# Performance work log

Measured on AMD Instinct MI355X. Metric: run time of the kernel, lower is better.

Reference implementation:

```python
import jax, jax.numpy as jnp
import numpy as np

ALPHA1 = 0.1
ALPHA2 = 0.1
NOISE = 0.02
B, T, H, O = 128, 512, 512, 3


def setup_inputs() -> dict:
    key = jax.random.key(0)
    ks = jax.random.split(key, 10)
    return {
        "x": jax.random.normal(ks[0], (B, T, 5), dtype=jnp.float32),
        "wi_stim": jax.random.normal(ks[1], (3, H), dtype=jnp.float32) / np.sqrt(3),
        "wrec11": jax.random.normal(ks[2], (H, H), dtype=jnp.float32) / np.sqrt(H),
        "wi_ctx": jax.random.normal(ks[3], (2, H), dtype=jnp.float32) / np.sqrt(2),
        "wrec22": jax.random.normal(ks[4], (H, H), dtype=jnp.float32) / np.sqrt(H),
        "wrec12": jax.random.normal(ks[5], (H, H), dtype=jnp.float32) / np.sqrt(H),
        "wrec21": jax.random.normal(ks[6], (H, H), dtype=jnp.float32) / np.sqrt(H),
        "wo": jax.random.normal(ks[7], (H, O), dtype=jnp.float32) / np.sqrt(H),
        "noise1": jax.random.normal(ks[8], (T, B, H), dtype=jnp.float32),
        "noise2": jax.random.normal(ks[9], (T, B, H), dtype=jnp.float32),
    }


def reference(x, wi_stim, wrec11, wi_ctx, wrec22, wrec12, wrec21, wo, noise1, noise2):
    # x: [B, T, 5]; noise: [T, B, H] (pre-sampled standard normals, scaled by NOISE)
    xs = jnp.transpose(x[:, :, :3], (1, 0, 2))  # [T, B, 3]
    xc = jnp.transpose(x[:, :, 3:], (1, 0, 2))  # [T, B, 2]

    def step(carry, inp):
        h1, h2 = carry
        xsi, xci, n1, n2 = inp
        h1 = (1 - ALPHA1) * h1 + ALPHA1 * (
            xsi @ wi_stim + jnp.tanh(h1) @ wrec11 + jnp.tanh(h2) @ wrec12 + n1 * NOISE
        )
        # note: h2 update uses the freshly-updated h1 (as in the torch loop)
        h2 = (1 - ALPHA2) * h2 + ALPHA2 * (
            xci @ wi_ctx + jnp.tanh(h1) @ wrec21 + jnp.tanh(h2) @ wrec22 + n2 * NOISE
        )
        return (h1, h2), jnp.tanh(h2) @ wo

    h0 = jnp.zeros((x.shape[0], wrec11.shape[0]), dtype=x.dtype)
    _, out_t = jax.lax.scan(step, (h0, h0), (xs, xc, noise1, noise2))  # [T, B, O]
    return jnp.transpose(out_t, (1, 0, 2))  # [B, T, O]
```

## Files before the change

kernel.cpp:

```cpp
#include <hip/hip_runtime.h>
#include <hip/hip_bf16.h>

#define TT 512
#define BB 128
#define HH 512
#define NGROUP 8
#define NSLICE 8
#define ALPHA 0.1f
#define NOISE_S 0.02f

typedef __attribute__((ext_vector_type(8))) short short8;
typedef __attribute__((ext_vector_type(8))) _Float16 half8;
typedef __attribute__((ext_vector_type(4))) float f32x4;

#define WPACK_CH 132096
#define PUB1_B (WPACK_CH * 16)
#define PUB2_B (PUB1_B + NGROUP * 16384)
#define FLAG_B (PUB2_B + NGROUP * 16384)

__device__ __forceinline__ unsigned short f2h(float f) {
  return __builtin_bit_cast(unsigned short, (_Float16)f);
}

__device__ __forceinline__ float fast_tanh(float x) {
  float e = __builtin_amdgcn_exp2f(x * 2.8853900817779268f);
  return 1.0f - 2.0f * __builtin_amdgcn_rcpf(e + 1.0f);
}

__device__ __forceinline__ f32x4 mfma16(short8 a, short8 b, f32x4 c) {
  return __builtin_amdgcn_mfma_f32_16x16x32_f16(
      __builtin_bit_cast(half8, a), __builtin_bit_cast(half8, b), c, 0, 0, 0);
}

__global__ void pack_weights(const float* __restrict__ w11, const float* __restrict__ w12,
                             const float* __restrict__ w21, const float* __restrict__ w22,
                             const float* __restrict__ wo, unsigned short* __restrict__ dst) {
  int idx = blockIdx.x * 256 + threadIdx.x;
  if (idx < 131072) {
    int which = idx >> 16;
    int c0 = idx & 65535;
    int kt = c0 >> 11, rem = c0 & 2047;
    int nt = rem >> 6, lane = rem & 63;
    const float* wlo = which ? w21 : w11;
    const float* whi = which ? w22 : w12;
    unsigned short* p = dst + (size_t)idx * 8;
    int n = nt * 16 + (lane & 15);
    int kb = kt * 32 + ((lane >> 4) & 3) * 8;
#pragma unroll
    for (int i = 0; i < 8; ++i) {
      int k = kb + i;
      float v = (k < HH) ? wlo[k * HH + n] : whi[(k - HH) * HH + n];
      p[i] = f2h(v);
    }
  } else if (idx < 132096) {
    int c0 = idx - 131072;
    int kt = c0 >> 6, lane = c0 & 63;
    unsigned short* p = dst + (size_t)131072 * 8 + (size_t)c0 * 8;
    int n = lane & 15;
    int kb = kt * 32 + ((lane >> 4) & 3) * 8;
#pragma unroll
    for (int i = 0; i < 8; ++i) {
      float v = (n < 3) ? wo[(kb + i) * 3 + n] : 0.0f;
      p[i] = f2h(v);
    }
  }
}

__global__ void zero_ws(int* __restrict__ p, int n) {
  for (int i = blockIdx.x * 256 + threadIdx.x; i < n; i += gridDim.x * 256)
    p[i] = 0;
}

__global__ __launch_bounds__(256, 1)
void rnn_main(const float* __restrict__ x, const float* __restrict__ wi_stim,
              const float* __restrict__ wi_ctx, const float* __restrict__ noise1,
              const float* __restrict__ noise2, char* __restrict__ ws,
              float* __restrict__ out) {
  __shared__ __align__(16) unsigned short T1buf[16 * 512];
  __shared__ __align__(16) unsigned short T2buf[16 * 512];
  __shared__ __align__(16) unsigned short WOlds[16 * 512];
  __shared__ float xstage[2][16][5];

  const int tid = threadIdx.x;
  const int w = tid >> 6, lane = tid & 63;
  const int c16 = lane & 15, kh = lane >> 4;
  const int g = blockIdx.x & (NGROUP - 1);
  const int slice = blockIdx.x >> 3;
  const int nt = slice * 4 + w;
  const int n0 = nt * 16;
  const int b0 = g * 16;
  const int lrow0 = kh * 4;

  const short8* __restrict__ WC = (const short8*)ws;
  unsigned short* __restrict__ pub1 = (unsigned short*)(ws + PUB1_B) + g * 8192;
  unsigned short* __restrict__ pub2 = (unsigned short*)(ws + PUB2_B) + g * 8192;
  int* __restrict__ fl1 = (int*)(ws + FLAG_B) + g * 8;
  int* __restrict__ fl2 = (int*)(ws + FLAG_B) + NGROUP * 8 + g * 8;

  short8 z = {0, 0, 0, 0, 0, 0, 0, 0};
  for (int i = tid; i < 1024; i += 256) {
    ((short8*)T1buf)[i] = z;
    ((short8*)T2buf)[i] = z;
  }
#pragma unroll
  for (int c = 0; c < 4; ++c) {
    int kt = w * 4 + c;
    short8 v = WC[131072 + kt * 64 + lane];
    *(short8*)&WOlds[kt * 512 + lane * 8] = v;
  }
  if (tid < 80) {
    int b = tid / 5, c = tid % 5;
    xstage[0][b][c] = x[((size_t)(b0 + b) * TT + 0) * 5 + c];
  }

  float wis[3], wic[2];
#pragma unroll
  for (int c = 0; c < 3; ++c) wis[c] = wi_stim[c * HH + n0 + c16];
#pragma unroll
  for (int c = 0; c < 2; ++c) wic[c] = wi_ctx[c * HH + n0 + c16];

  float h1[4] = {0, 0, 0, 0}, h2[4] = {0, 0, 0, 0};

  const int kt_p = nt >> 1;
  const int hi = (((nt & 1) * 16) + c16) >> 3;
  const int ci = c16 & 7;

  const short8* __restrict__ WAp = WC + nt * 64 + lane;
  const short8* __restrict__ WBp = WC + 65536 + nt * 64 + lane;

  auto poll = [&](int* f, int target) {
    int v;
    do {
      v = (lane < 8) ? __hip_atomic_load(&f[lane], __ATOMIC_RELAXED,
                                         __HIP_MEMORY_SCOPE_AGENT)
                     : target;
    } while (!__all(v >= target));
    __builtin_amdgcn_sched_barrier(0);
    asm volatile("" ::: "memory");
  };

  __syncthreads();

  for (int t = 0; t < TT; ++t) {
    const int buf = t & 1;

    float n1v[4];
#pragma unroll
    for (int r = 0; r < 4; ++r)
      n1v[r] = noise1[((size_t)t * BB + b0 + lrow0 + r) * HH + n0 + c16];

    f32x4 aA = {0, 0, 0, 0}, aB = {0, 0, 0, 0};
#pragma unroll
    for (int kt = 0; kt < 16; ++kt) {
      short8 a1 = *(const short8*)&T1buf[kt * 512 + lane * 8];
      aA = mfma16(a1, WAp[kt * 2048], aA);
    }
    poll(fl2, t);
#pragma unroll
    for (int c = 0; c < 4; ++c) {
      int kt = w * 4 + c;
      const unsigned long long* src =
          (const unsigned long long*)&pub2[kt * 512 + lane * 8];
      unsigned long long v0 = __hip_atomic_load(&src[0], __ATOMIC_RELAXED,
                                                __HIP_MEMORY_SCOPE_AGENT);
      unsigned long long v1 = __hip_atomic_load(&src[1], __ATOMIC_RELAXED,
                                                __HIP_MEMORY_SCOPE_AGENT);
      *(unsigned long long*)&T2buf[kt * 512 + lane * 8] = v0;
      *(unsigned long long*)&T2buf[kt * 512 + lane * 8 + 4] = v1;
    }
    __syncthreads();
#pragma unroll
    for (int kt = 0; kt < 16; ++kt) {
      short8 a2 = *(const short8*)&T2buf[kt * 512 + lane * 8];
      aB = mfma16(a2, WAp[(16 + kt) * 2048], aB);
    }

    if (t > 0 && slice == ((t - 1) & 7) && w == 0) {
      f32x4 ao = {0, 0, 0, 0};
#pragma unroll
      for (int kt = 0; kt < 16; ++kt) {
        short8 a2 = *(const short8*)&T2buf[kt * 512 + lane * 8];
        short8 bo = *(const short8*)&WOlds[kt * 512 + lane * 8];
        ao = mfma16(a2, bo, ao);
      }
      if (c16 < 3) {
#pragma unroll
        for (int r = 0; r < 4; ++r)
          out[((size_t)(b0 + lrow0 + r) * TT + (t - 1)) * 3 + c16] = ao[r];
      }
    }

    unsigned short tp[4];
#pragma unroll
    for (int r = 0; r < 4; ++r) {
      float pre = aA[r] + aB[r]
                + wis[0] * xstage[buf][lrow0 + r][0]
                + wis[1] * xstage[buf][lrow0 + r][1]
                + wis[2] * xstage[buf][lrow0 + r][2]
                + NOISE_S * n1v[r];
      float h = (1.0f - ALPHA) * h1[r] + ALPHA * pre;
      h1[r] = h;
      tp[r] = f2h(fast_tanh(h));
    }
#pragma unroll
    for (int r = 0; r < 4; ++r)
      __hip_atomic_store(&pub1[kt_p * 512 + (lrow0 + r + hi * 16) * 8 + ci], tp[r],
                         __ATOMIC_RELAXED, __HIP_MEMORY_SCOPE_AGENT);
    asm volatile("s_waitcnt vmcnt(0)" ::: "memory");
    __syncthreads();
    if (tid == 0)
      __hip_atomic_store(&fl1[slice], t + 1, __ATOMIC_RELAXED,
                         __HIP_MEMORY_SCOPE_AGENT);

    float n2v[4];
#pragma unroll
    for (int r = 0; r < 4; ++r)
      n2v[r] = noise2[((size_t)t * BB + b0 + lrow0 + r) * HH + n0 + c16];

    f32x4 bA = {0, 0, 0, 0}, bB = {0, 0, 0, 0};
#pragma unroll
    for (int kt = 0; kt < 16; ++kt) {
      short8 a2 = *(const short8*)&T2buf[kt * 512 + lane * 8];
      bB = mfma16(a2, WBp[(16 + kt) * 2048], bB);
    }
    poll(fl1, t + 1);
#pragma unroll
    for (int c = 0; c < 4; ++c) {
      int kt = w * 4 + c;
      const unsigned long long* src =
          (const unsigned long long*)&pub1[kt * 512 + lane * 8];
      unsigned long long v0 = __hip_atomic_load(&src[0], __ATOMIC_RELAXED,
                                                __HIP_MEMORY_SCOPE_AGENT);
      unsigned long long v1 = __hip_atomic_load(&src[1], __ATOMIC_RELAXED,
                                                __HIP_MEMORY_SCOPE_AGENT);
      *(unsigned long long*)&T1buf[kt * 512 + lane * 8] = v0;
      *(unsigned long long*)&T1buf[kt * 512 + lane * 8 + 4] = v1;
    }
    if (t + 1 < TT && tid < 80) {
      int b = tid / 5, c = tid % 5;
      xstage[buf ^ 1][b][c] = x[((size_t)(b0 + b) * TT + (t + 1)) * 5 + c];
    }
    __syncthreads();
#pragma unroll
    for (int kt = 0; kt < 16; ++kt) {
      short8 a1 = *(const short8*)&T1buf[kt * 512 + lane * 8];
      bA = mfma16(a1, WBp[kt * 2048], bA);
    }
#pragma unroll
    for (int r = 0; r < 4; ++r) {
      float pre = bA[r] + bB[r]
                + wic[0] * xstage[buf][lrow0 + r][3]
                + wic[1] * xstage[buf][lrow0 + r][4]
                + NOISE_S * n2v[r];
      float h = (1.0f - ALPHA) * h2[r] + ALPHA * pre;
      h2[r] = h;
      tp[r] = f2h(fast_tanh(h));
    }
#pragma unroll
    for (int r = 0; r < 4; ++r)
      __hip_atomic_store(&pub2[kt_p * 512 + (lrow0 + r + hi * 16) * 8 + ci], tp[r],
                         __ATOMIC_RELAXED, __HIP_MEMORY_SCOPE_AGENT);
    asm volatile("s_waitcnt vmcnt(0)" ::: "memory");
    __syncthreads();
    if (tid == 0)
      __hip_atomic_store(&fl2[slice], t + 1, __ATOMIC_RELAXED,
                         __HIP_MEMORY_SCOPE_AGENT);
  }

  if (slice == ((TT - 1) & 7)) {
    poll(fl2, TT);
#pragma unroll
    for (int c = 0; c < 4; ++c) {
      int kt = w * 4 + c;
      const unsigned long long* src =
          (const unsigned long long*)&pub2[kt * 512 + lane * 8];
      unsigned long long v0 = __hip_atomic_load(&src[0], __ATOMIC_RELAXED,
                                                __HIP_MEMORY_SCOPE_AGENT);
      unsigned long long v1 = __hip_atomic_load(&src[1], __ATOMIC_RELAXED,
                                                __HIP_MEMORY_SCOPE_AGENT);
      *(unsigned long long*)&T2buf[kt * 512 + lane * 8] = v0;
      *(unsigned long long*)&T2buf[kt * 512 + lane * 8 + 4] = v1;
    }
    __syncthreads();
    if (w == 0) {
      f32x4 ao = {0, 0, 0, 0};
#pragma unroll
      for (int kt = 0; kt < 16; ++kt) {
        short8 a2 = *(const short8*)&T2buf[kt * 512 + lane * 8];
        short8 bo = *(const short8*)&WOlds[kt * 512 + lane * 8];
        ao = mfma16(a2, bo, ao);
      }
      if (c16 < 3) {
#pragma unroll
        for (int r = 0; r < 4; ++r)
          out[((size_t)(b0 + lrow0 + r) * TT + (TT - 1)) * 3 + c16] = ao[r];
      }
    }
  }
}

extern "C" void kernel_launch(void* const* d_in, const int* in_sizes, int n_in,
                              void* d_out, int out_size, void* d_ws, size_t ws_size,
                              hipStream_t stream) {
  const float* x       = (const float*)d_in[0];
  const float* wi_stim = (const float*)d_in[1];
  const float* w11     = (const float*)d_in[2];
  const float* wi_ctx  = (const float*)d_in[3];
  const float* w22     = (const float*)d_in[4];
  const float* w12     = (const float*)d_in[5];
  const float* w21     = (const float*)d_in[6];
  const float* wo      = (const float*)d_in[7];
  const float* n1      = (const float*)d_in[8];
  const float* n2      = (const float*)d_in[9];
  char* ws = (char*)d_ws;

  int nz = (NGROUP * 16384 * 2 + 2 * NGROUP * 8 * 4) / 4;
  zero_ws<<<64, 256, 0, stream>>>((int*)(ws + PUB1_B), nz);
  pack_weights<<<516, 256, 0, stream>>>(w11, w12, w21, w22, wo,
                                        (unsigned short*)ws);
  rnn_main<<<NSLICE * NGROUP, 256, 0, stream>>>(x, wi_stim, wi_ctx, n1, n2, ws,
                                                (float*)d_out);
}
```

Before: 3.745 ms.

## Tag published hidden states with step counters and keep weights in registers

Each published fp16 tanh value now goes into a 32-bit word together with a step tag. Consumers poll the data words themselves until every tag reaches the expected step, then unpack the values into LDS. This removes the separate flag stores, the vmcnt waits and the extra __syncthreads on the producer side, and adds wider polling traffic in exchange. The recurrent weight fragments (64 short8 per thread) are also loaded once into registers rather than re-read from global memory every step. That may raise register pressure heavily and risk spills.

```diff
diff --git a/kernel.cpp b/kernel.cpp
--- a/kernel.cpp
+++ b/kernel.cpp
@@ -15,8 +15,7 @@
 
 #define WPACK_CH 132096
 #define PUB1_B (WPACK_CH * 16)
-#define PUB2_B (PUB1_B + NGROUP * 16384)
-#define FLAG_B (PUB2_B + NGROUP * 16384)
+#define PUB2_B (PUB1_B + NGROUP * 32768)
 
 __device__ __forceinline__ unsigned short f2h(float f) {
   return __builtin_bit_cast(unsigned short, (_Float16)f);
@@ -92,10 +91,8 @@
   const int lrow0 = kh * 4;
 
   const short8* __restrict__ WC = (const short8*)ws;
-  unsigned short* __restrict__ pub1 = (unsigned short*)(ws + PUB1_B) + g * 8192;
-  unsigned short* __restrict__ pub2 = (unsigned short*)(ws + PUB2_B) + g * 8192;
-  int* __restrict__ fl1 = (int*)(ws + FLAG_B) + g * 8;
-  int* __restrict__ fl2 = (int*)(ws + FLAG_B) + NGROUP * 8 + g * 8;
+  unsigned* __restrict__ pub1 = (unsigned*)(ws + PUB1_B) + g * 8192;
+  unsigned* __restrict__ pub2 = (unsigned*)(ws + PUB2_B) + g * 8192;
 
   short8 z = {0, 0, 0, 0, 0, 0, 0, 0};
   for (int i = tid; i < 1024; i += 256) {
@@ -113,6 +110,18 @@
     xstage[0][b][c] = x[((size_t)(b0 + b) * TT + 0) * 5 + c];
   }
 
+  short8 wA[32], wB[32];
+#pragma unroll
+  for (int kt = 0; kt < 32; ++kt) {
+    wA[kt] = WC[kt * 2048 + nt * 64 + lane];
+    wB[kt] = WC[65536 + kt * 2048 + nt * 64 + lane];
+  }
+#pragma unroll
+  for (int kt = 0; kt < 32; ++kt) {
+    asm volatile("" : "+v"(wA[kt]));
+    asm volatile("" : "+v"(wB[kt]));
+  }
+
   float wis[3], wic[2];
 #pragma unroll
   for (int c = 0; c < 3; ++c) wis[c] = wi_stim[c * HH + n0 + c16];
@@ -125,24 +134,46 @@
   const int hi = (((nt & 1) * 16) + c16) >> 3;
   const int ci = c16 & 7;
 
-  const short8* __restrict__ WAp = WC + nt * 64 + lane;
-  const short8* __restrict__ WBp = WC + 65536 + nt * 64 + lane;
-
-  auto poll = [&](int* f, int target) {
-    int v;
+  auto stage_poll = [&](const unsigned* pubw, unsigned short* Tbuf, unsigned exp) {
+    unsigned long long v[4][4];
+    bool ok;
     do {
-      v = (lane < 8) ? __hip_atomic_load(&f[lane], __ATOMIC_RELAXED,
-                                         __HIP_MEMORY_SCOPE_AGENT)
-                     : target;
-    } while (!__all(v >= target));
+      ok = true;
+#pragma unroll
+      for (int c = 0; c < 4; ++c) {
+        const unsigned long long* src =
+            (const unsigned long long*)(pubw + ((w * 4 + c) << 9)) + lane * 4;
+#pragma unroll
+        for (int j = 0; j < 4; ++j) {
+          v[c][j] = __hip_atomic_load(&src[j], __ATOMIC_RELAXED,
+                                      __HIP_MEMORY_SCOPE_AGENT);
+          ok &= (((unsigned)(v[c][j] >> 16) & 0xffffu) >= exp);
+          ok &= ((unsigned)(v[c][j] >> 48) >= exp);
+        }
+      }
+    } while (!ok);
     __builtin_amdgcn_sched_barrier(0);
     asm volatile("" ::: "memory");
+#pragma unroll
+    for (int c = 0; c < 4; ++c) {
+      unsigned long long u0 = (v[c][0] & 0xffffull)
+                            | (((v[c][0] >> 32) & 0xffffull) << 16)
+                            | ((v[c][1] & 0xffffull) << 32)
+                            | (((v[c][1] >> 32) & 0xffffull) << 48);
+      unsigned long long u1 = (v[c][2] & 0xffffull)
+                            | (((v[c][2] >> 32) & 0xffffull) << 16)
+                            | ((v[c][3] & 0xffffull) << 32)
+                            | (((v[c][3] >> 32) & 0xffffull) << 48);
+      *(unsigned long long*)&Tbuf[(w * 4 + c) * 512 + lane * 8] = u0;
+      *(unsigned long long*)&Tbuf[(w * 4 + c) * 512 + lane * 8 + 4] = u1;
+    }
   };
 
   __syncthreads();
 
   for (int t = 0; t < TT; ++t) {
     const int buf = t & 1;
+    const unsigned tagA = (unsigned)(t + 1) << 16;
 
     float n1v[4];
 #pragma unroll
@@ -153,26 +184,14 @@
 #pragma unroll
     for (int kt = 0; kt < 16; ++kt) {
       short8 a1 = *(const short8*)&T1buf[kt * 512 + lane * 8];
-      aA = mfma16(a1, WAp[kt * 2048], aA);
-    }
-    poll(fl2, t);
-#pragma unroll
-    for (int c = 0; c < 4; ++c) {
-      int kt = w * 4 + c;
-      const unsigned long long* src =
-          (const unsigned long long*)&pub2[kt * 512 + lane * 8];
-      unsigned long long v0 = __hip_atomic_load(&src[0], __ATOMIC_RELAXED,
-                                                __HIP_MEMORY_SCOPE_AGENT);
-      unsigned long long v1 = __hip_atomic_load(&src[1], __ATOMIC_RELAXED,
-                                                __HIP_MEMORY_SCOPE_AGENT);
-      *(unsigned long long*)&T2buf[kt * 512 + lane * 8] = v0;
-      *(unsigned long long*)&T2buf[kt * 512 + lane * 8 + 4] = v1;
-    }
+      aA = mfma16(a1, wA[kt], aA);
+    }
+    stage_poll(pub2, T2buf, (unsigned)t);
     __syncthreads();
 #pragma unroll
     for (int kt = 0; kt < 16; ++kt) {
       short8 a2 = *(const short8*)&T2buf[kt * 512 + lane * 8];
-      aB = mfma16(a2, WAp[(16 + kt) * 2048], aB);
+      aB = mfma16(a2, wA[16 + kt], aB);
     }
 
     if (t > 0 && slice == ((t - 1) & 7) && w == 0) {
@@ -204,13 +223,8 @@
     }
 #pragma unroll
     for (int r = 0; r < 4; ++r)
-      __hip_atomic_store(&pub1[kt_p * 512 + (lrow0 + r + hi * 16) * 8 + ci], tp[r],
-                         __ATOMIC_RELAXED, __HIP_MEMORY_SCOPE_AGENT);
-    asm volatile("s_waitcnt vmcnt(0)" ::: "memory");
-    __syncthreads();
-    if (tid == 0)
-      __hip_atomic_store(&fl1[slice], t + 1, __ATOMIC_RELAXED,
-                         __HIP_MEMORY_SCOPE_AGENT);
+      __hip_atomic_store(&pub1[kt_p * 512 + (lrow0 + r + hi * 16) * 8 + ci],
+                         tagA | tp[r], __ATOMIC_RELAXED, __HIP_MEMORY_SCOPE_AGENT);
 
     float n2v[4];
 #pragma unroll
@@ -221,21 +235,9 @@
 #pragma unroll
     for (int kt = 0; kt < 16; ++kt) {
       short8 a2 = *(const short8*)&T2buf[kt * 512 + lane * 8];
-      bB = mfma16(a2, WBp[(16 + kt) * 2048], bB);
-    }
-    poll(fl1, t + 1);
-#pragma unroll
-    for (int c = 0; c < 4; ++c) {
-      int kt = w * 4 + c;
-      const unsigned long long* src =
-          (const unsigned long long*)&pub1[kt * 512 + lane * 8];
-      unsigned long long v0 = __hip_atomic_load(&src[0], __ATOMIC_RELAXED,
-                                                __HIP_MEMORY_SCOPE_AGENT);
-      unsigned long long v1 = __hip_atomic_load(&src[1], __ATOMIC_RELAXED,
-                                                __HIP_MEMORY_SCOPE_AGENT);
-      *(unsigned long long*)&T1buf[kt * 512 + lane * 8] = v0;
-      *(unsigned long long*)&T1buf[kt * 512 + lane * 8 + 4] = v1;
-    }
+      bB = mfma16(a2, wB[16 + kt], bB);
+    }
+    stage_poll(pub1, T1buf, (unsigned)(t + 1));
     if (t + 1 < TT && tid < 80) {
       int b = tid / 5, c = tid % 5;
       xstage[buf ^ 1][b][c] = x[((size_t)(b0 + b) * TT + (t + 1)) * 5 + c];
@@ -244,7 +246,7 @@
 #pragma unroll
     for (int kt = 0; kt < 16; ++kt) {
       short8 a1 = *(const short8*)&T1buf[kt * 512 + lane * 8];
-      bA = mfma16(a1, WBp[kt * 2048], bA);
+      bA = mfma16(a1, wB[kt], bA);
     }
 #pragma unroll
     for (int r = 0; r < 4; ++r) {
@@ -258,29 +260,12 @@
     }
 #pragma unroll
     for (int r = 0; r < 4; ++r)
-      __hip_atomic_store(&pub2[kt_p * 512 + (lrow0 + r + hi * 16) * 8 + ci], tp[r],
-                         __ATOMIC_RELAXED, __HIP_MEMORY_SCOPE_AGENT);
-    asm volatile("s_waitcnt vmcnt(0)" ::: "memory");
-    __syncthreads();
-    if (tid == 0)
-      __hip_atomic_store(&fl2[slice], t + 1, __ATOMIC_RELAXED,
-                         __HIP_MEMORY_SCOPE_AGENT);
+      __hip_atomic_store(&pub2[kt_p * 512 + (lrow0 + r + hi * 16) * 8 + ci],
+                         tagA | tp[r], __ATOMIC_RELAXED, __HIP_MEMORY_SCOPE_AGENT);
   }
 
   if (slice == ((TT - 1) & 7)) {
-    poll(fl2, TT);
-#pragma unroll
-    for (int c = 0; c < 4; ++c) {
-      int kt = w * 4 + c;
-      const unsigned long long* src =
-          (const unsigned long long*)&pub2[kt * 512 + lane * 8];
-      unsigned long long v0 = __hip_atomic_load(&src[0], __ATOMIC_RELAXED,
-                                                __HIP_MEMORY_SCOPE_AGENT);
-      unsigned long long v1 = __hip_atomic_load(&src[1], __ATOMIC_RELAXED,
-                                                __HIP_MEMORY_SCOPE_AGENT);
-      *(unsigned long long*)&T2buf[kt * 512 + lane * 8] = v0;
-      *(unsigned long long*)&T2buf[kt * 512 + lane * 8 + 4] = v1;
-    }
+    stage_poll(pub2, T2buf, (unsigned)TT);
     __syncthreads();
     if (w == 0) {
       f32x4 ao = {0, 0, 0, 0};
@@ -314,7 +299,7 @@
   const float* n2      = (const float*)d_in[9];
   char* ws = (char*)d_ws;
 
-  int nz = (NGROUP * 16384 * 2 + 2 * NGROUP * 8 * 4) / 4;
+  int nz = (NGROUP * 32768 * 2) / 4;
   zero_ws<<<64, 256, 0, stream>>>((int*)(ws + PUB1_B), nz);
   pack_weights<<<516, 256, 0, stream>>>(w11, w12, w21, w22, wo,
                                         (unsigned short*)ws);
```

New measurement: 3.578 ms. -4.5%, faster.
